# Kernel optimization log

Measured on AMD Instinct MI355X. Metric: run time of the kernel, lower is better.

## Reference

```python
import jax, jax.numpy as jnp
import numpy as np

N = 16384      # number of points (pixels)
C = 64         # value channels of U
D_REF = 5      # bilateral reference feature dim (xy + rgb)


def setup_inputs() -> dict:
    key = jax.random.key(0)
    k1, k2 = jax.random.split(key)
    U = jax.random.normal(k1, (N, C), dtype=jnp.float32)
    ref = jax.random.normal(k2, (N, D_REF), dtype=jnp.float32)
    return {"U": U, "ref": ref}


def reference(U, ref):
    # Gaussian filtering on reference features (exact form of the LSH-approx filter):
    #   out[i] = sum_j exp(-0.5 * ||ref_i - ref_j||^2) * U[j]  -  U[i]
    sq = jnp.sum(ref * ref, axis=-1)                      # [N]
    d2 = sq[:, None] + sq[None, :] - 2.0 * (ref @ ref.T)  # [N, N] squared distances
    K = jnp.exp(-0.5 * jnp.maximum(d2, 0.0))              # [N, N] Gaussian kernel
    return K @ U - U                                       # [N, C]
```

## Files before the change

### kernel.cpp

```cpp
#include <hip/hip_runtime.h>
#include <hip/hip_bf16.h>
#include <stdint.h>

#define N_PTS 16384
#define C_CH  64
#define D_REF 5
#define LOG2E 1.44269504088896340736f
#define JSPLIT 8
#define IBLOCKS 128
#define CHUNKS 16

typedef __attribute__((ext_vector_type(8))) short bf16x8;
typedef __attribute__((ext_vector_type(4))) float f32x4;

__device__ __forceinline__ unsigned short bf16rn(float v) {
    unsigned u = __builtin_bit_cast(unsigned, v) + 0x8000u;
    return (unsigned short)(u >> 16);
}
__device__ __forceinline__ float bf16tof(unsigned short h) {
    unsigned u = ((unsigned)h) << 16;
    return __builtin_bit_cast(float, u);
}
__device__ __forceinline__ unsigned pack2bf16(float lo, float hi) {
    unsigned a = __builtin_bit_cast(unsigned, lo) + 0x8000u;
    unsigned b = __builtin_bit_cast(unsigned, hi) + 0x8000u;
    return __builtin_amdgcn_perm(b, a, 0x07060302u);
}
__device__ __forceinline__ float fast_exp2(float x) {
#if __has_builtin(__builtin_amdgcn_exp2f)
    return __builtin_amdgcn_exp2f(x);
#else
    return exp2f(x);
#endif
}

__device__ __forceinline__ void dma16(const unsigned short* g, unsigned short* l) {
#if __has_builtin(__builtin_amdgcn_global_load_lds)
    __builtin_amdgcn_global_load_lds(
        (const __attribute__((address_space(1))) unsigned int*)g,
        (__attribute__((address_space(3))) unsigned int*)l, 16, 0, 0);
#else
    const int lane = threadIdx.x & 63;
    *(uint4*)(l + lane * 8) = *(const uint4*)(g);
#endif
}

__global__ __launch_bounds__(256) void prep_all(
    const float* __restrict__ U, const float* __restrict__ ref,
    unsigned short* __restrict__ packA, unsigned short* __restrict__ packB,
    unsigned short* __restrict__ utPack)
{
    __shared__ unsigned short tile[64 * 80];
    const int bid = blockIdx.x;
    const int t   = threadIdx.x;

    if (bid < 512) {
        const int gid  = bid * 256 + t;
        const int half = gid >> 16;
        const int id   = gid & 0xFFFF;
        const int tile16 = id >> 6;
        const int lane = id & 63;
        const int q    = lane >> 4;
        const int m    = lane & 15;
        const int p    = tile16 * 16 + m;

        const float* r = ref + (size_t)p * D_REF;
        float rv[5];
        float sq = 0.f;
#pragma unroll
        for (int d = 0; d < 5; ++d) { rv[d] = r[d]; sq += rv[d] * rv[d]; }
        const float h = -0.5f * LOG2E * sq;

        unsigned short bh[5], bl[5];
#pragma unroll
        for (int d = 0; d < 5; ++d) {
            const float base = half ? rv[d] * LOG2E : rv[d];
            bh[d] = bf16rn(base);
            bl[d] = bf16rn(base - bf16tof(bh[d]));
        }
        const unsigned short hh  = bf16rn(h);
        const unsigned short hl  = bf16rn(h - bf16tof(hh));
        const unsigned short one = 0x3F80;

        unsigned short outv[8];
#pragma unroll
        for (int tt = 0; tt < 8; ++tt) {
            const int k = q * 8 + tt;
            unsigned short v = 0;
            if (!half) {
                if      (k < 5)   v = bh[k];
                else if (k < 10)  v = bh[k - 5];
                else if (k < 15)  v = bl[k - 10];
                else if (k == 15) v = hh;
                else if (k == 16) v = hl;
                else if (k <= 18) v = one;
            } else {
                if      (k < 5)   v = bh[k];
                else if (k < 10)  v = bl[k - 5];
                else if (k < 15)  v = bh[k - 10];
                else if (k <= 16) v = one;
                else if (k == 17) v = hh;
                else if (k == 18) v = hl;
            }
            outv[tt] = v;
        }
        unsigned short* dst = (half ? packB : packA) + ((size_t)tile16 * 64 + lane) * 8;
        *(uint4*)dst = *(uint4*)outv;
    } else {
        const int b  = bid - 512;
        const int j0 = b * 64;
        const int c  = t & 63;
        const int jb = t >> 6;
#pragma unroll
        for (int k = 0; k < 16; ++k) {
            const int jr = jb + k * 4;
            tile[c * 80 + jr] = bf16rn(U[(size_t)(j0 + jr) * C_CH + c]);
        }
        __syncthreads();
#pragma unroll
        for (int rep = 0; rep < 2; ++rep) {
            const int id   = rep * 256 + t;
            const int lane = id & 63;
            const int ct   = (id >> 6) & 3;
            const int kt   = id >> 8;
            const int m    = lane & 15;
            const int q    = lane >> 4;
            const int cc   = ct * 16 + m;
            const int jloc = kt * 32 + q * 8;
            const uint4 frag = *(const uint4*)&tile[cc * 80 + jloc];
            const int jtile  = b * 2 + kt;
            *(uint4*)&utPack[(((size_t)jtile * 4 + ct) * 64 + lane) * 8] = frag;
        }
    }
}

__global__ __launch_bounds__(256, 4) void lsh_main(
    const float* __restrict__ U,
    const unsigned short* __restrict__ packA,
    const unsigned short* __restrict__ packB,
    const unsigned short* __restrict__ utPack,
    float* __restrict__ part,
    float* __restrict__ out,
    int use_part)
{
    __shared__ __align__(16) unsigned short sh[16384];

    const int t    = threadIdx.x;
    const int lane = t & 63;
    const int wave = t >> 6;
    const int q    = lane >> 4;
    const int m    = lane & 15;

    const int ib = blockIdx.x >> 3;
    const int js = blockIdx.x & 7;

    bf16x8 bfrag[2];
#pragma unroll
    for (int s = 0; s < 2; ++s) {
        const int itile = ib * 8 + wave * 2 + s;
        bfrag[s] = *(const bf16x8*)(packB + ((size_t)itile * 64 + lane) * 8);
    }

    f32x4 acc[2][4];
#pragma unroll
    for (int s = 0; s < 2; ++s)
#pragma unroll
        for (int ct = 0; ct < 4; ++ct) acc[s][ct] = (f32x4){0.f, 0.f, 0.f, 0.f};

    unsigned short* sW = sh + 12288 + wave * 1024;
    const int sWr0 = (q >> 1) * 128 + m * 8 + (q & 1) * 4;

    for (int chunk = 0; chunk < CHUNKS; ++chunk) {
        const unsigned short* srcU = utPack + (size_t)(js * 64 + chunk * 4) * 2048;
        const unsigned short* srcA = packA  + (size_t)(js * 128 + chunk * 8) * 512;
        __syncthreads();
#pragma unroll
        for (int r = 0; r < 4; ++r)
            dma16(srcU + r * 2048 + wave * 512 + lane * 8, sh + r * 2048 + wave * 512);
#pragma unroll
        for (int r = 0; r < 2; ++r)
            dma16(srcA + r * 2048 + wave * 512 + lane * 8, sh + 8192 + r * 2048 + wave * 512);
        __syncthreads();

#pragma unroll
        for (int kt = 0; kt < 4; ++kt) {
            const bf16x8 ga0 = *(const bf16x8*)(sh + 8192 + (kt * 2 + 0) * 512 + lane * 8);
            const bf16x8 ga1 = *(const bf16x8*)(sh + 8192 + (kt * 2 + 1) * 512 + lane * 8);
            bf16x8 uf[4];
#pragma unroll
            for (int ct = 0; ct < 4; ++ct)
                uf[ct] = *(const bf16x8*)(sh + kt * 2048 + ct * 512 + lane * 8);

            const f32x4 z = (f32x4){0.f, 0.f, 0.f, 0.f};
            f32x4 g0[2], g1[2];
#pragma unroll
            for (int s = 0; s < 2; ++s) {
                g0[s] = __builtin_amdgcn_mfma_f32_16x16x32_bf16(ga0, bfrag[s], z, 0, 0, 0);
                g1[s] = __builtin_amdgcn_mfma_f32_16x16x32_bf16(ga1, bfrag[s], z, 0, 0, 0);
            }
#pragma unroll
            for (int s = 0; s < 2; ++s) {
                float e0[4], e1[4];
#pragma unroll
                for (int r2 = 0; r2 < 4; ++r2) {
                    e0[r2] = fast_exp2(g0[s][r2]);
                    e1[r2] = fast_exp2(g1[s][r2]);
                }
                uint2 w0 = { pack2bf16(e0[0], e0[1]), pack2bf16(e0[2], e0[3]) };
                uint2 w1 = { pack2bf16(e1[0], e1[1]), pack2bf16(e1[2], e1[3]) };
                unsigned short* sb = sW + s * 512;
                *(uint2*)&sb[sWr0]       = w0;
                *(uint2*)&sb[sWr0 + 256] = w1;
            }
#pragma unroll
            for (int s = 0; s < 2; ++s) {
                const bf16x8 sf = *(const bf16x8*)&sW[s * 512 + lane * 8];
#pragma unroll
                for (int ct = 0; ct < 4; ++ct)
                    acc[s][ct] = __builtin_amdgcn_mfma_f32_16x16x32_bf16(
                        uf[ct], sf, acc[s][ct], 0, 0, 0);
            }
        }
    }

    if (use_part) {
        float* dst = part + ((size_t)js * IBLOCKS + ib) * (128 * C_CH);
#pragma unroll
        for (int s = 0; s < 2; ++s) {
            const int i_loc = (wave * 2 + s) * 16 + m;
#pragma unroll
            for (int ct = 0; ct < 4; ++ct)
                *(f32x4*)(dst + i_loc * C_CH + ct * 16 + q * 4) = acc[s][ct];
        }
    } else {
#pragma unroll
        for (int s = 0; s < 2; ++s) {
            const int i_glob = ib * 128 + (wave * 2 + s) * 16 + m;
#pragma unroll
            for (int ct = 0; ct < 4; ++ct)
#pragma unroll
                for (int r2 = 0; r2 < 4; ++r2) {
                    const int c = ct * 16 + q * 4 + r2;
                    float val = acc[s][ct][r2];
                    if (js == 0) val -= U[(size_t)i_glob * C_CH + c];
                    atomicAdd(&out[(size_t)i_glob * C_CH + c], val);
                }
        }
    }
}

__global__ __launch_bounds__(256) void reduce_part(
    const f32x4* __restrict__ part, const f32x4* __restrict__ U,
    f32x4* __restrict__ out)
{
    const int x = blockIdx.x * 256 + threadIdx.x;
    f32x4 s = part[x];
#pragma unroll
    for (int js = 1; js < JSPLIT; ++js)
        s += part[((size_t)js << 18) + x];
    out[x] = s - U[x];
}

extern "C" void kernel_launch(void* const* d_in, const int* in_sizes, int n_in,
                              void* d_out, int out_size, void* d_ws, size_t ws_size,
                              hipStream_t stream) {
    const float* U   = (const float*)d_in[0];
    const float* ref = (const float*)d_in[1];
    float* out = (float*)d_out;

    unsigned short* utPack = (unsigned short*)d_ws;
    unsigned short* packA  = (unsigned short*)((char*)d_ws + (size_t)2 * 1024 * 1024);
    unsigned short* packB  = (unsigned short*)((char*)d_ws + (size_t)3 * 1024 * 1024);
    float*          part   = (float*)((char*)d_ws + (size_t)4 * 1024 * 1024);

    const size_t need = (size_t)(4 + 4 * JSPLIT) * 1024 * 1024;
    const int use_part = (ws_size >= need) ? 1 : 0;

    if (!use_part)
        hipMemsetAsync(d_out, 0, (size_t)out_size * sizeof(float), stream);

    prep_all<<<768, 256, 0, stream>>>(U, ref, packA, packB, utPack);
    lsh_main<<<IBLOCKS * JSPLIT, 256, 0, stream>>>(U, packA, packB, utPack,
                                                   part, out, use_part);
    if (use_part)
        reduce_part<<<1024, 256, 0, stream>>>((const f32x4*)part, (const f32x4*)U,
                                              (f32x4*)out);
}
```

Baseline: 128.6 us.

## Keep exp weights in registers via permuted packA layout and double i-tile per wave

Reorders the rows of the packA operand so the MFMA output fragment of the Gaussian-weight GEMM lines up with the B-operand layout of the second GEMM. The exp weights can then be packed straight into registers instead of going through an LDS round trip. Each wave now covers four i-tiles instead of two, so each U fragment loaded from LDS feeds more MFMAs, and the j-split is raised to 16 when the workspace allows. The cost is higher register pressure (16 accumulators and 4 exp fragments per wave), a larger partial buffer, and more reduction traffic.

```diff
diff --git a/kernel.cpp b/kernel.cpp
--- a/kernel.cpp
+++ b/kernel.cpp
@@ -6,9 +6,7 @@
 #define C_CH  64
 #define D_REF 5
 #define LOG2E 1.44269504088896340736f
-#define JSPLIT 8
-#define IBLOCKS 128
-#define CHUNKS 16
+#define IBLOCKS 64
 
 typedef __attribute__((ext_vector_type(8))) short bf16x8;
 typedef __attribute__((ext_vector_type(4))) float f32x4;
@@ -62,7 +60,8 @@
         const int lane = id & 63;
         const int q    = lane >> 4;
         const int m    = lane & 15;
-        const int p    = tile16 * 16 + m;
+        const int p = half ? (tile16 * 16 + m)
+                           : ((tile16 >> 1) * 32 + (m >> 2) * 8 + (m & 3) + (tile16 & 1) * 4);
 
         const float* r = ref + (size_t)p * D_REF;
         float rv[5];
@@ -134,6 +133,7 @@
     }
 }
 
+template<int JS>
 __global__ __launch_bounds__(256, 4) void lsh_main(
     const float* __restrict__ U,
     const unsigned short* __restrict__ packA,
@@ -143,7 +143,8 @@
     float* __restrict__ out,
     int use_part)
 {
-    __shared__ __align__(16) unsigned short sh[16384];
+    constexpr int CHUNKS = (N_PTS / JS) / 128;
+    __shared__ __align__(16) unsigned short sh[12288];
 
     const int t    = threadIdx.x;
     const int lane = t & 63;
@@ -151,28 +152,25 @@
     const int q    = lane >> 4;
     const int m    = lane & 15;
 
-    const int ib = blockIdx.x >> 3;
-    const int js = blockIdx.x & 7;
-
-    bf16x8 bfrag[2];
-#pragma unroll
-    for (int s = 0; s < 2; ++s) {
-        const int itile = ib * 8 + wave * 2 + s;
+    const int ib = blockIdx.x / JS;
+    const int js = blockIdx.x % JS;
+
+    bf16x8 bfrag[4];
+#pragma unroll
+    for (int s = 0; s < 4; ++s) {
+        const int itile = ib * 16 + wave * 4 + s;
         bfrag[s] = *(const bf16x8*)(packB + ((size_t)itile * 64 + lane) * 8);
     }
 
-    f32x4 acc[2][4];
-#pragma unroll
-    for (int s = 0; s < 2; ++s)
+    f32x4 acc[4][4];
+#pragma unroll
+    for (int s = 0; s < 4; ++s)
 #pragma unroll
         for (int ct = 0; ct < 4; ++ct) acc[s][ct] = (f32x4){0.f, 0.f, 0.f, 0.f};
 
-    unsigned short* sW = sh + 12288 + wave * 1024;
-    const int sWr0 = (q >> 1) * 128 + m * 8 + (q & 1) * 4;
-
     for (int chunk = 0; chunk < CHUNKS; ++chunk) {
-        const unsigned short* srcU = utPack + (size_t)(js * 64 + chunk * 4) * 2048;
-        const unsigned short* srcA = packA  + (size_t)(js * 128 + chunk * 8) * 512;
+        const unsigned short* srcU = utPack + (size_t)(js * CHUNKS + chunk) * 8192;
+        const unsigned short* srcA = packA  + (size_t)(js * CHUNKS + chunk) * 4096;
         __syncthreads();
 #pragma unroll
         for (int r = 0; r < 4; ++r)
@@ -186,56 +184,44 @@
         for (int kt = 0; kt < 4; ++kt) {
             const bf16x8 ga0 = *(const bf16x8*)(sh + 8192 + (kt * 2 + 0) * 512 + lane * 8);
             const bf16x8 ga1 = *(const bf16x8*)(sh + 8192 + (kt * 2 + 1) * 512 + lane * 8);
-            bf16x8 uf[4];
-#pragma unroll
-            for (int ct = 0; ct < 4; ++ct)
-                uf[ct] = *(const bf16x8*)(sh + kt * 2048 + ct * 512 + lane * 8);
 
             const f32x4 z = (f32x4){0.f, 0.f, 0.f, 0.f};
-            f32x4 g0[2], g1[2];
-#pragma unroll
-            for (int s = 0; s < 2; ++s) {
-                g0[s] = __builtin_amdgcn_mfma_f32_16x16x32_bf16(ga0, bfrag[s], z, 0, 0, 0);
-                g1[s] = __builtin_amdgcn_mfma_f32_16x16x32_bf16(ga1, bfrag[s], z, 0, 0, 0);
+            bf16x8 sfrag[4];
+#pragma unroll
+            for (int s = 0; s < 4; ++s) {
+                const f32x4 g0 = __builtin_amdgcn_mfma_f32_16x16x32_bf16(ga0, bfrag[s], z, 0, 0, 0);
+                const f32x4 g1 = __builtin_amdgcn_mfma_f32_16x16x32_bf16(ga1, bfrag[s], z, 0, 0, 0);
+                union { unsigned u[4]; bf16x8 v; } sb;
+                sb.u[0] = pack2bf16(fast_exp2(g0[0]), fast_exp2(g0[1]));
+                sb.u[1] = pack2bf16(fast_exp2(g0[2]), fast_exp2(g0[3]));
+                sb.u[2] = pack2bf16(fast_exp2(g1[0]), fast_exp2(g1[1]));
+                sb.u[3] = pack2bf16(fast_exp2(g1[2]), fast_exp2(g1[3]));
+                sfrag[s] = sb.v;
             }
 #pragma unroll
-            for (int s = 0; s < 2; ++s) {
-                float e0[4], e1[4];
-#pragma unroll
-                for (int r2 = 0; r2 < 4; ++r2) {
-                    e0[r2] = fast_exp2(g0[s][r2]);
-                    e1[r2] = fast_exp2(g1[s][r2]);
-                }
-                uint2 w0 = { pack2bf16(e0[0], e0[1]), pack2bf16(e0[2], e0[3]) };
-                uint2 w1 = { pack2bf16(e1[0], e1[1]), pack2bf16(e1[2], e1[3]) };
-                unsigned short* sb = sW + s * 512;
-                *(uint2*)&sb[sWr0]       = w0;
-                *(uint2*)&sb[sWr0 + 256] = w1;
+            for (int ct = 0; ct < 4; ++ct) {
+                const bf16x8 uf = *(const bf16x8*)(sh + kt * 2048 + ct * 512 + lane * 8);
+#pragma unroll
+                for (int s = 0; s < 4; ++s)
+                    acc[s][ct] = __builtin_amdgcn_mfma_f32_16x16x32_bf16(
+                        uf, sfrag[s], acc[s][ct], 0, 0, 0);
             }
-#pragma unroll
-            for (int s = 0; s < 2; ++s) {
-                const bf16x8 sf = *(const bf16x8*)&sW[s * 512 + lane * 8];
-#pragma unroll
-                for (int ct = 0; ct < 4; ++ct)
-                    acc[s][ct] = __builtin_amdgcn_mfma_f32_16x16x32_bf16(
-                        uf[ct], sf, acc[s][ct], 0, 0, 0);
-            }
         }
     }
 
     if (use_part) {
-        float* dst = part + ((size_t)js * IBLOCKS + ib) * (128 * C_CH);
-#pragma unroll
-        for (int s = 0; s < 2; ++s) {
-            const int i_loc = (wave * 2 + s) * 16 + m;
+        float* dst = part + ((size_t)js * IBLOCKS + ib) * (256 * C_CH);
+#pragma unroll
+        for (int s = 0; s < 4; ++s) {
+            const int i_loc = (wave * 4 + s) * 16 + m;
 #pragma unroll
             for (int ct = 0; ct < 4; ++ct)
                 *(f32x4*)(dst + i_loc * C_CH + ct * 16 + q * 4) = acc[s][ct];
         }
     } else {
 #pragma unroll
-        for (int s = 0; s < 2; ++s) {
-            const int i_glob = ib * 128 + (wave * 2 + s) * 16 + m;
+        for (int s = 0; s < 4; ++s) {
+            const int i_glob = ib * 256 + (wave * 4 + s) * 16 + m;
 #pragma unroll
             for (int ct = 0; ct < 4; ++ct)
 #pragma unroll
@@ -249,6 +235,7 @@
     }
 }
 
+template<int JS>
 __global__ __launch_bounds__(256) void reduce_part(
     const f32x4* __restrict__ part, const f32x4* __restrict__ U,
     f32x4* __restrict__ out)
@@ -256,7 +243,7 @@
     const int x = blockIdx.x * 256 + threadIdx.x;
     f32x4 s = part[x];
 #pragma unroll
-    for (int js = 1; js < JSPLIT; ++js)
+    for (int js = 1; js < JS; ++js)
         s += part[((size_t)js << 18) + x];
     out[x] = s - U[x];
 }
@@ -273,16 +260,22 @@
     unsigned short* packB  = (unsigned short*)((char*)d_ws + (size_t)3 * 1024 * 1024);
     float*          part   = (float*)((char*)d_ws + (size_t)4 * 1024 * 1024);
 
-    const size_t need = (size_t)(4 + 4 * JSPLIT) * 1024 * 1024;
-    const int use_part = (ws_size >= need) ? 1 : 0;
-
-    if (!use_part)
+    const size_t MB = 1024 * 1024;
+    prep_all<<<768, 256, 0, stream>>>(U, ref, packA, packB, utPack);
+
+    if (ws_size >= (4 + 4 * 16) * MB) {
+        lsh_main<16><<<IBLOCKS * 16, 256, 0, stream>>>(U, packA, packB, utPack,
+                                                       part, out, 1);
+        reduce_part<16><<<1024, 256, 0, stream>>>((const f32x4*)part,
+                                                  (const f32x4*)U, (f32x4*)out);
+    } else if (ws_size >= (4 + 4 * 8) * MB) {
+        lsh_main<8><<<IBLOCKS * 8, 256, 0, stream>>>(U, packA, packB, utPack,
+                                                     part, out, 1);
+        reduce_part<8><<<1024, 256, 0, stream>>>((const f32x4*)part,
+                                                 (const f32x4*)U, (f32x4*)out);
+    } else {
         hipMemsetAsync(d_out, 0, (size_t)out_size * sizeof(float), stream);
-
-    prep_all<<<768, 256, 0, stream>>>(U, ref, packA, packB, utPack);
-    lsh_main<<<IBLOCKS * JSPLIT, 256, 0, stream>>>(U, packA, packB, utPack,
-                                                   part, out, use_part);
-    if (use_part)
-        reduce_part<<<1024, 256, 0, stream>>>((const f32x4*)part, (const f32x4*)U,
-                                              (f32x4*)out);
-}
+        lsh_main<8><<<IBLOCKS * 8, 256, 0, stream>>>(U, packA, packB, utPack,
+                                                     part, out, 0);
+    }
+}
```

Result: no change. 126.5 us (-1.6%).
